# Performance work log

Hardware: AMD Instinct MI355X
Metric: run time of the kernel (lower is better)

Reference implementation:

```python
import jax, jax.numpy as jnp
import numpy as np

EPS = 1e-8

def unit_projection(x):
    # project each embedding vector so its Fourier coefficients have unit magnitude
    f = jnp.fft.fft(x, axis=-1)
    f = f / jnp.maximum(jnp.abs(f), EPS)
    return jnp.real(jnp.fft.ifft(f, axis=-1))

def bind(a, b):
    return jnp.fft.irfft(jnp.fft.rfft(a, axis=-1) * jnp.fft.rfft(b, axis=-1), n=a.shape[-1], axis=-1)

def unbind(s, k):
    # k is unit-magnitude in Fourier domain, so its inverse is its conjugate
    return jnp.fft.irfft(jnp.fft.rfft(s, axis=-1) * jnp.conj(jnp.fft.rfft(k, axis=-1)), n=s.shape[-1], axis=-1)

def layer_norm(x, g, b):
    mu = jnp.mean(x, axis=-1, keepdims=True)
    var = jnp.var(x, axis=-1, keepdims=True)
    return (x - mu) * jax.lax.rsqrt(var + 1e-5) * g + b

def setup_inputs():
    key = jax.random.key(0)
    ks = jax.random.split(key, 12)
    B, S, D = 4, 2048, 1024
    sc = 1.0 / np.sqrt(D)
    inp = {
        'x': jax.random.normal(ks[0], (B, S, D), jnp.float32),
        'Wq': jax.random.normal(ks[1], (D, D), jnp.float32) * sc,
        'bq': jnp.zeros((D,), jnp.float32),
        'Wk': jax.random.normal(ks[2], (D, D), jnp.float32) * sc,
        'bk': jnp.zeros((D,), jnp.float32),
        'Wv': jax.random.normal(ks[3], (D, D), jnp.float32) * sc,
        'bv': jnp.zeros((D,), jnp.float32),
        'ln1_g': jnp.ones((D,), jnp.float32), 'ln1_b': jnp.zeros((D,), jnp.float32),
        'ln2_g': jnp.ones((D,), jnp.float32), 'ln2_b': jnp.zeros((D,), jnp.float32),
        'W1': jax.random.normal(ks[4], (D, 4 * D), jnp.float32) * sc,
        'b1': jnp.zeros((4 * D,), jnp.float32),
        'W2': jax.random.normal(ks[5], (4 * D, D), jnp.float32) * (1.0 / np.sqrt(4 * D)),
        'b2': jnp.zeros((D,), jnp.float32),
    }
    return inp

def reference(x, Wq, bq, Wk, bk, Wv, bv, ln1_g, ln1_b, ln2_g, ln2_b, W1, b1, W2, b2):
    h = layer_norm(x, ln1_g, ln1_b)
    q = unit_projection(h @ Wq + bq)
    k = unit_projection(h @ Wk + bk)
    v = unit_projection(h @ Wv + bv)
    s = jnp.cumsum(bind(k, v), axis=1)  # causal prefix-sum over sequence
    mixed = unbind(s, q)
    x = x + mixed  # dropout=0.0
    h2 = layer_norm(x, ln2_g, ln2_b)
    mlp = jax.nn.gelu(h2 @ W1 + b1, approximate=False) @ W2 + b2
    return x + mlp
```

## Files before the change

### kernel.cpp

```cpp
#include <hip/hip_runtime.h>
#include <cstdint>
#include <cstddef>

#define DD 1024
#define SSEQ 2048
#define NB 4
#define MROWS 8192
#define FBINS 513
#define FPAD 520
#define WFP 1152
#define NQKV 3456
#define NHID 4096
#define NCHUNK 64
#define SCHUNK 32

typedef _Float16 f16_t;
typedef _Float16 f16x8 __attribute__((ext_vector_type(8)));
typedef _Float16 f16x2 __attribute__((ext_vector_type(2)));
typedef float f32x4 __attribute__((ext_vector_type(4)));

__device__ __forceinline__ float2 cmul(float2 a, float2 b) {
  return make_float2(a.x * b.x - a.y * b.y, a.x * b.y + a.y * b.x);
}

__device__ __forceinline__ void async_cp16(const void* g, void* l) {
  __builtin_amdgcn_global_load_lds(
      (const __attribute__((address_space(1))) void*)g,
      (__attribute__((address_space(3))) void*)l, 16, 0, 0);
}

template <int N> __device__ __forceinline__ void vwait();
template <> __device__ __forceinline__ void vwait<0>() { asm volatile("s_waitcnt vmcnt(0)" ::: "memory"); }
template <> __device__ __forceinline__ void vwait<1>() { asm volatile("s_waitcnt vmcnt(1)" ::: "memory"); }
template <> __device__ __forceinline__ void vwait<2>() { asm volatile("s_waitcnt vmcnt(2)" ::: "memory"); }
template <> __device__ __forceinline__ void vwait<3>() { asm volatile("s_waitcnt vmcnt(3)" ::: "memory"); }
template <> __device__ __forceinline__ void vwait<4>() { asm volatile("s_waitcnt vmcnt(4)" ::: "memory"); }

__device__ __forceinline__ float fast_gelu(float val) {
  float av = __builtin_fabsf(val);
  float z = av * 0.70710678118654752f;
  float t = __builtin_amdgcn_rcpf(__builtin_fmaf(0.3275911f, z, 1.0f));
  float poly = t * __builtin_fmaf(t,
      __builtin_fmaf(t, __builtin_fmaf(t,
          __builtin_fmaf(t, 1.061405429f, -1.453152027f),
          1.421413741f), -0.284496736f), 0.254829592f);
  float e = __builtin_amdgcn_exp2f(z * z * -1.4426950408889634f);
  float w = poly * e;
  float r = fmaxf(val, 0.0f);
  return __builtin_fmaf(-0.5f * av, w, r);
}

__device__ __forceinline__ void fft1024(float2* bufA, float2* bufB,
                                        const float2* tw, int tid) {
  float2* s = bufA;
  float2* d = bufB;
  for (int m = 1; m < 1024; m <<= 1) {
#pragma unroll
    for (int r2 = 0; r2 < 2; ++r2) {
      int u = tid + r2 * 256;
      int k = u & (m - 1);
      int jm = u - k;
      float2 c0 = s[u];
      float2 c1 = s[u + 512];
      float2 wt = tw[jm];
      float2 su = make_float2(c0.x + c1.x, c0.y + c1.y);
      float2 df = make_float2(c0.x - c1.x, c0.y - c1.y);
      float2 pr = cmul(wt, df);
      d[2 * jm + k] = su;
      d[2 * jm + k + m] = pr;
    }
    __syncthreads();
    float2* tmp = s; s = d; d = tmp;
  }
}

__device__ __forceinline__ float2* fft512(float2* bufA, float2* bufB,
                                          const float2* tw, int tid) {
  float2* s = bufA;
  float2* d = bufB;
  for (int m = 1; m < 512; m <<= 1) {
    int u = tid;
    int k = u & (m - 1);
    int jm = u - k;
    float2 c0 = s[u];
    float2 c1 = s[u + 256];
    float2 wt = tw[jm];
    float2 su = make_float2(c0.x + c1.x, c0.y + c1.y);
    float2 df = make_float2(c0.x - c1.x, c0.y - c1.y);
    float2 pr = cmul(wt, df);
    d[2 * jm + k] = su;
    d[2 * jm + k + m] = pr;
    __syncthreads();
    float2* tmp = s; s = d; d = tmp;
  }
  return s;
}

__global__ __launch_bounds__(256) void wfft_k(
    const float* __restrict__ Wq, const float* __restrict__ Wk,
    const float* __restrict__ Wv, float* __restrict__ WfAll) {
  __shared__ float2 tw[512];
  __shared__ float2 bufA[1024];
  __shared__ float2 bufB[1024];
  const int tid = threadIdx.x;
  const int p = blockIdx.x >> 10, k = blockIdx.x & 1023;
  const float* W = (p == 0) ? Wq : ((p == 1) ? Wk : Wv);
  for (int t = tid; t < 512; t += 256) {
    float ang = -6.2831853071795864769f * (float)t * (1.0f / 1024.0f);
    tw[t] = make_float2(cosf(ang), sinf(ang));
  }
  const float* src = W + (size_t)k * DD;
  for (int t = tid; t < 1024; t += 256) bufA[t] = make_float2(src[t], 0.f);
  __syncthreads();
  fft1024(bufA, bufB, tw, tid);
  float* dst = WfAll + ((size_t)p * DD + k) * WFP;
  for (int t = tid; t <= 512; t += 256) {
    float2 f = bufA[t];
    dst[2 * t] = f.x;
    dst[2 * t + 1] = f.y;
  }
  for (int j = 1026 + tid; j < WFP; j += 256) dst[j] = 0.f;
}

__global__ __launch_bounds__(256) void bfft_k(
    const float* __restrict__ bq, const float* __restrict__ bk,
    const float* __restrict__ bv, float* __restrict__ biasC) {
  __shared__ float2 tw[512];
  __shared__ float2 bufA[1024];
  __shared__ float2 bufB[1024];
  const int tid = threadIdx.x;
  const int p = blockIdx.x;
  const float* bsrc = (p == 0) ? bq : ((p == 1) ? bk : bv);
  for (int t = tid; t < 512; t += 256) {
    float ang = -6.2831853071795864769f * (float)t * (1.0f / 1024.0f);
    tw[t] = make_float2(cosf(ang), sinf(ang));
  }
  for (int t = tid; t < 1024; t += 256) bufA[t] = make_float2(bsrc[t], 0.f);
  __syncthreads();
  fft1024(bufA, bufB, tw, tid);
  float* dst = biasC + (size_t)p * WFP;
  for (int t = tid; t <= 512; t += 256) {
    float2 f = bufA[t];
    dst[2 * t] = f.x;
    dst[2 * t + 1] = f.y;
  }
  for (int j = 1026 + tid; j < WFP; j += 256) dst[j] = 0.f;
}

__global__ __launch_bounds__(256) void transpose_cast_k(
    const float* __restrict__ W, f16_t* __restrict__ Wt, int K, int N) {
  __shared__ float tile[32][33];
  const int tx = threadIdx.x & 31, ty = threadIdx.x >> 5;
  const int n0 = blockIdx.x * 32, k0 = blockIdx.y * 32;
#pragma unroll
  for (int i = 0; i < 32; i += 8)
    tile[ty + i][tx] = W[(size_t)(k0 + ty + i) * N + n0 + tx];
  __syncthreads();
#pragma unroll
  for (int i = 0; i < 32; i += 8)
    Wt[(size_t)(n0 + ty + i) * K + k0 + tx] = (f16_t)tile[tx][ty + i];
}

__global__ __launch_bounds__(256) void ln_cast2_k(
    const float* __restrict__ x, const float* __restrict__ g,
    const float* __restrict__ b, f16_t* __restrict__ hH,
    f16_t* __restrict__ hL) {
  const int row = blockIdx.x, tid = threadIdx.x;
  __shared__ float red[8];
  const float* xr = x + (size_t)row * DD;
  float v[4], ls = 0.f, lq = 0.f;
#pragma unroll
  for (int i = 0; i < 4; ++i) {
    v[i] = xr[i * 256 + tid];
    ls += v[i];
    lq += v[i] * v[i];
  }
#pragma unroll
  for (int o = 32; o > 0; o >>= 1) {
    ls += __shfl_down(ls, o);
    lq += __shfl_down(lq, o);
  }
  const int lane = tid & 63, w = tid >> 6;
  if (lane == 0) { red[w] = ls; red[w + 4] = lq; }
  __syncthreads();
  const float S = red[0] + red[1] + red[2] + red[3];
  const float Q = red[4] + red[5] + red[6] + red[7];
  const float mean = S * (1.f / 1024.f);
  const float var = Q * (1.f / 1024.f) - mean * mean;
  const float rs = rsqrtf(var + 1e-5f);
#pragma unroll
  for (int i = 0; i < 4; ++i) {
    int n = i * 256 + tid;
    float val = (v[i] - mean) * rs * g[n] + b[n];
    f16_t hi = (f16_t)val;
    hH[(size_t)row * DD + n] = hi;
    hL[(size_t)row * DD + n] = (f16_t)(val - (float)hi);
  }
}

template <int RHALF>
__device__ __forceinline__ void stage_half(const f16_t* __restrict__ G,
                                           int grow0, int ldk, int kt,
                                           f16_t* ls, int w, int lane) {
  const int srow = lane >> 3;
  const int slot = lane & 7;
#pragma unroll
  for (int j = 0; j < RHALF / 64; ++j) {
    const int rb = (w + j * 8) * 8;
    const int row = rb + srow;
    const int gg = (slot - (row & 7)) & 7;
    async_cp16(G + (size_t)(grow0 + row) * ldk + kt + gg * 8, ls + rb * 64);
  }
}

template <int BM, int BN>
__device__ __forceinline__ void readA(const f16_t* As, int mq, int wm, int lane,
                                      f16x8 (&aR)[BM / 64][2]) {
#pragma unroll
  for (int mf = 0; mf < BM / 64; ++mf) {
    const int m = mq * (BM / 2) + wm * (BM / 4) + mf * 16 + (lane & 15);
#pragma unroll
    for (int ks = 0; ks < 2; ++ks) {
      const int cg = ks * 4 + (lane >> 4);
      const int sl = (cg + (m & 7)) & 7;
      aR[mf][ks] = *(const f16x8*)(As + m * 64 + sl * 8);
    }
  }
}

template <int BM, int BN>
__device__ __forceinline__ void readB(const f16_t* Bs, int nq, int wn, int lane,
                                      f16x8 (&bR)[BN / 128][2]) {
#pragma unroll
  for (int nf = 0; nf < BN / 128; ++nf) {
    const int n = nq * (BN / 2) + wn * (BN / 8) + nf * 16 + (lane & 15);
#pragma unroll
    for (int ks = 0; ks < 2; ++ks) {
      const int cg = ks * 4 + (lane >> 4);
      const int sl = (cg + (n & 7)) & 7;
      bR[nf][ks] = *(const f16x8*)(Bs + n * 64 + sl * 8);
    }
  }
}

template <int MF, int NF>
__device__ __forceinline__ void mfma_q(f32x4 (&acc)[MF][NF],
                                       const f16x8 (&aR)[MF][2],
                                       const f16x8 (&bR)[NF][2]) {
#pragma unroll
  for (int ks = 0; ks < 2; ++ks)
#pragma unroll
    for (int mf = 0; mf < MF; ++mf)
#pragma unroll
      for (int nf = 0; nf < NF; ++nf)
        acc[mf][nf] = __builtin_amdgcn_mfma_f32_16x16x32_f16(
            aR[mf][ks], bR[nf][ks], acc[mf][nf], 0, 0, 0);
}

template <int BM, int BN, int MM, int NN, int KK, int EPI>
__global__ __launch_bounds__(512, 2) void gemm8p_k(
    const f16_t* __restrict__ A, const f16_t* __restrict__ Bt,
    const float* __restrict__ bias, const float* __restrict__ resid,
    float* __restrict__ outF, f16_t* __restrict__ outH) {
  constexpr int MF = BM / 64;
  constexpr int NF = BN / 128;
  constexpr int LA = BM / 128;
  constexpr int LB = BN / 128;
  constexpr int NT = KK / 64;
  constexpr int TILE = (BM + BN) * 64;
  __shared__ alignas(16) f16_t lds[2 * TILE];

  const int tid = threadIdx.x;
  const int lane = tid & 63;
  const int w = tid >> 6;
  const int wm = w >> 2;
  const int wn = w & 3;

  constexpr int ntm = MM / BM, ntn = NN / BN;
  constexpr int per = (ntm * ntn) / 8;
  const int lin = (int)blockIdx.x;
  const int s = (lin & 7) * per + (lin >> 3);
  const int bn = (s % ntn) * BN;
  const int bm = (s / ntn) * BM;

  f32x4 acc[2][2][MF][NF];
#pragma unroll
  for (int a0 = 0; a0 < 2; ++a0)
#pragma unroll
    for (int a1 = 0; a1 < 2; ++a1)
#pragma unroll
      for (int mf = 0; mf < MF; ++mf)
#pragma unroll
        for (int nf = 0; nf < NF; ++nf)
          acc[a0][a1][mf][nf] = (f32x4){0.f, 0.f, 0.f, 0.f};

  {
    f16_t* A0s = lds;
    f16_t* B0s = lds + BM * 64;
    stage_half<BM / 2>(A, bm, KK, 0, A0s, w, lane);
    stage_half<BN / 2>(Bt, bn, KK, 0, B0s, w, lane);
    stage_half<BN / 2>(Bt, bn + BN / 2, KK, 0, B0s + (BN / 2) * 64, w, lane);
    stage_half<BM / 2>(A, bm + BM / 2, KK, 0, A0s + (BM / 2) * 64, w, lane);
  }
  vwait<LA + LB>();
  __builtin_amdgcn_s_barrier();

  f16x8 aR[MF][2], bR0[NF][2], bR1[NF][2];

  for (int t = 0; t < NT; ++t) {
    const int cur = t & 1;
    f16_t* As = lds + cur * TILE;
    f16_t* Bs = As + BM * 64;
    f16_t* Asn = lds + (cur ^ 1) * TILE;
    f16_t* Bsn = Asn + BM * 64;
    const bool pre = (t + 1 < NT);
    const int ktn = (t + 1) << 6;

    readA<BM, BN>(As, 0, wm, lane, aR);
    readB<BM, BN>(Bs, 0, wn, lane, bR0);
    if (pre) stage_half<BM / 2>(A, bm, KK, ktn, Asn, w, lane);
    __builtin_amdgcn_s_barrier();
    __builtin_amdgcn_s_setprio(1);
    mfma_q<MF, NF>(acc[0][0], aR, bR0);
    __builtin_amdgcn_s_setprio(0);
    if (pre) vwait<2 * LA>(); else vwait<LA>();
    __builtin_amdgcn_s_barrier();

    readB<BM, BN>(Bs, 1, wn, lane, bR1);
    if (pre) stage_half<BN / 2>(Bt, bn, KK, ktn, Bsn, w, lane);
    __builtin_amdgcn_s_barrier();
    __builtin_amdgcn_s_setprio(1);
    mfma_q<MF, NF>(acc[0][1], aR, bR1);
    __builtin_amdgcn_s_setprio(0);
    if (pre) vwait<LA + LB>(); else vwait<0>();
    __builtin_amdgcn_s_barrier();

    readA<BM, BN>(As, 1, wm, lane, aR);
    if (pre) stage_half<BN / 2>(Bt, bn + BN / 2, KK, ktn,
                                Bsn + (BN / 2) * 64, w, lane);
    __builtin_amdgcn_s_barrier();
    __builtin_amdgcn_s_setprio(1);
    mfma_q<MF, NF>(acc[1][0], aR, bR0);
    __builtin_amdgcn_s_setprio(0);
    __builtin_amdgcn_s_barrier();

    if (pre) stage_half<BM / 2>(A, bm + BM / 2, KK, ktn,
                                Asn + (BM / 2) * 64, w, lane);
    __builtin_amdgcn_s_barrier();
    __builtin_amdgcn_s_setprio(1);
    mfma_q<MF, NF>(acc[1][1], aR, bR1);
    __builtin_amdgcn_s_setprio(0);
    if (pre) vwait<LA + LB>();
    __builtin_amdgcn_s_barrier();
  }

  const int q4 = lane >> 4;
  const int cn = lane & 15;
#pragma unroll
  for (int mq = 0; mq < 2; ++mq)
#pragma unroll
    for (int nq = 0; nq < 2; ++nq)
#pragma unroll
      for (int mf = 0; mf < MF; ++mf)
#pragma unroll
        for (int nf = 0; nf < NF; ++nf) {
          const int gcol = bn + nq * (BN / 2) + wn * (BN / 8) + nf * 16 + cn;
          const float bv = bias[gcol];
          const int grow0 = bm + mq * (BM / 2) + wm * (BM / 4) + mf * 16 + q4 * 4;
#pragma unroll
          for (int i = 0; i < 4; ++i) {
            const float val = acc[mq][nq][mf][nf][i] + bv;
            const size_t idx = (size_t)(grow0 + i) * NN + gcol;
            if (EPI == 1) {
              outH[idx] = (f16_t)fast_gelu(val);
            } else {
              outF[idx] = val + resid[idx];
            }
          }
        }
}

__global__ __launch_bounds__(512, 2) void gemm_qkv8p_k(
    const f16_t* __restrict__ Ahi, const f16_t* __restrict__ Alo,
    const f16_t* __restrict__ Bt, const float* __restrict__ bias,
    float* __restrict__ outF) {
  constexpr int BM = 256, BN = 128;
  constexpr int MF = 4, NF = 1;
  constexpr int LA = 2, LB = 1;
  constexpr int TILE = (BM + BN) * 64;
  __shared__ alignas(16) f16_t lds[2 * TILE];

  const int tid = threadIdx.x;
  const int lane = tid & 63;
  const int w = tid >> 6;
  const int wm = w >> 2, wn = w & 3;

  const int lin = (int)blockIdx.x;
  const int xcd = lin & 7, idx = lin >> 3;
  int bm, bn;
  bool qmode;
  if (idx < 36) {
    const int h = xcd * 36 + idx;
    bm = (h / 9) * 256;
    bn = (h % 9) * 128;
    qmode = true;
  } else {
    const int l = xcd * 72 + (idx - 36);
    bm = (l / 18) * 256;
    bn = 1152 + (l % 18) * 128;
    qmode = false;
  }
  const int NT = qmode ? 32 : 16;

  f32x4 acc[2][2][MF][NF];
#pragma unroll
  for (int a0 = 0; a0 < 2; ++a0)
#pragma unroll
    for (int a1 = 0; a1 < 2; ++a1)
#pragma unroll
      for (int mf = 0; mf < MF; ++mf)
#pragma unroll
        for (int nf = 0; nf < NF; ++nf)
          acc[a0][a1][mf][nf] = (f32x4){0.f, 0.f, 0.f, 0.f};

  {
    f16_t* A0s = lds;
    f16_t* B0s = lds + BM * 64;
    stage_half<BM / 2>(Ahi, bm, DD, 0, A0s, w, lane);
    stage_half<BN / 2>(Bt, bn, DD, 0, B0s, w, lane);
    stage_half<BN / 2>(Bt, bn + BN / 2, DD, 0, B0s + (BN / 2) * 64, w, lane);
    stage_half<BM / 2>(Ahi, bm + BM / 2, DD, 0, A0s + (BM / 2) * 64, w, lane);
  }
  vwait<LA + LB>();
  __builtin_amdgcn_s_barrier();

  f16x8 aR[MF][2], bR0[NF][2], bR1[NF][2];

  for (int t = 0; t < NT; ++t) {
    const int cur = t & 1;
    f16_t* As = lds + cur * TILE;
    f16_t* Bs = As + BM * 64;
    f16_t* Asn = lds + (cur ^ 1) * TILE;
    f16_t* Bsn = Asn + BM * 64;
    const bool pre = (t + 1 < NT);
    const int tt = t + 1;
    const f16_t* An = (qmode && tt >= 16) ? Alo : Ahi;
    const int ktn = (tt & 15) << 6;

    readA<BM, BN>(As, 0, wm, lane, aR);
    readB<BM, BN>(Bs, 0, wn, lane, bR0);
    if (pre) stage_half<BM / 2>(An, bm, DD, ktn, Asn, w, lane);
    __builtin_amdgcn_s_barrier();
    __builtin_amdgcn_s_setprio(1);
    mfma_q<MF, NF>(acc[0][0], aR, bR0);
    __builtin_amdgcn_s_setprio(0);
    if (pre) vwait<2 * LA>(); else vwait<LA>();
    __builtin_amdgcn_s_barrier();

    readB<BM, BN>(Bs, 1, wn, lane, bR1);
    if (pre) stage_half<BN / 2>(Bt, bn, DD, ktn, Bsn, w, lane);
    __builtin_amdgcn_s_barrier();
    __builtin_amdgcn_s_setprio(1);
    mfma_q<MF, NF>(acc[0][1], aR, bR1);
    __builtin_amdgcn_s_setprio(0);
    if (pre) vwait<LA + LB>(); else vwait<0>();
    __builtin_amdgcn_s_barrier();

    readA<BM, BN>(As, 1, wm, lane, aR);
    if (pre) stage_half<BN / 2>(Bt, bn + BN / 2, DD, ktn,
                                Bsn + (BN / 2) * 64, w, lane);
    __builtin_amdgcn_s_barrier();
    __builtin_amdgcn_s_setprio(1);
    mfma_q<MF, NF>(acc[1][0], aR, bR0);
    __builtin_amdgcn_s_setprio(0);
    __builtin_amdgcn_s_barrier();

    if (pre) stage_half<BM / 2>(An, bm + BM / 2, DD, ktn,
                                Asn + (BM / 2) * 64, w, lane);
    __builtin_amdgcn_s_barrier();
    __builtin_amdgcn_s_setprio(1);
    mfma_q<MF, NF>(acc[1][1], aR, bR1);
    __builtin_amdgcn_s_setprio(0);
    if (pre) vwait<LA + LB>();
    __builtin_amdgcn_s_barrier();
  }

  const int q4 = lane >> 4;
  const int cn = lane & 15;
#pragma unroll
  for (int mq = 0; mq < 2; ++mq)
#pragma unroll
    for (int nq = 0; nq < 2; ++nq)
#pragma unroll
      for (int mf = 0; mf < MF; ++mf)
#pragma unroll
        for (int nf = 0; nf < NF; ++nf) {
          const int gcol = bn + nq * (BN / 2) + wn * (BN / 8) + nf * 16 + cn;
          const float bv = bias[gcol];
          const int grow0 = bm + mq * (BM / 2) + wm * (BM / 4) + mf * 16 + q4 * 4;
#pragma unroll
          for (int i = 0; i < 4; ++i) {
            const size_t oidx = (size_t)(grow0 + i) * NQKV + gcol;
            outF[oidx] = acc[mq][nq][mf][nf][i] + bv;
          }
        }
}

__device__ __forceinline__ float2 unitc(float2 a) {
  float inv = 1.0f / fmaxf(sqrtf(a.x * a.x + a.y * a.y), 1e-8f);
  return make_float2(a.x * inv, a.y * inv);
}
__device__ __forceinline__ float2 bind_bin(const float2* r, int f) {
  float2 kn = unitc(r[576 + f]);
  float2 vn = unitc(r[1152 + f]);
  return cmul(kn, vn);
}

__global__ __launch_bounds__(256) void scan_pass1_k(
    const float* __restrict__ qkvF, float2* __restrict__ T) {
  const int bid = blockIdx.x;
  const int sc = bid & 63;
  const int fh = (bid >> 6) & 1;
  const int b = bid >> 7;
  const int s0 = sc * SCHUNK;
  const float2* base = (const float2*)(qkvF + ((size_t)(b * SSEQ + s0)) * NQKV);
  for (int f = fh * 256 + threadIdx.x; f < FBINS; f += 512) {
    float2 acc = make_float2(0.f, 0.f);
    const float2* r = base;
    for (int i = 0; i < SCHUNK; ++i) {
      float2 pv = bind_bin(r, f);
      acc.x += pv.x; acc.y += pv.y;
      r += NQKV / 2;
    }
    T[((size_t)b * NCHUNK + sc) * FBINS + f] = acc;
  }
}

__global__ void scan_pass2_k(float2* __restrict__ T) {
  const int idx = blockIdx.x * 256 + threadIdx.x;
  if (idx >= NB * FBINS) return;
  const int b = idx / FBINS, f = idx % FBINS;
  float2 acc = make_float2(0.f, 0.f);
  for (int sc = 0; sc < NCHUNK; ++sc) {
    size_t a = ((size_t)b * NCHUNK + sc) * FBINS + f;
    float2 v = T[a];
    T[a] = acc;
    acc.x += v.x; acc.y += v.y;
  }
}

__global__ __launch_bounds__(256) void scan_pass3_k(
    const float* __restrict__ qkvF, const float2* __restrict__ T,
    float2* __restrict__ Scum) {
  const int bid = blockIdx.x;
  const int sc = bid & 63;
  const int fh = (bid >> 6) & 1;
  const int b = bid >> 7;
  const int s0 = sc * SCHUNK;
  const float2* base = (const float2*)(qkvF + ((size_t)(b * SSEQ + s0)) * NQKV);
  for (int f = fh * 256 + threadIdx.x; f < FBINS; f += 512) {
    float2 acc = T[((size_t)b * NCHUNK + sc) * FBINS + f];
    const float2* r = base;
    size_t orow = ((size_t)(b * SSEQ + s0)) * FPAD + f;
    for (int i = 0; i < SCHUNK; ++i) {
      float2 pv = bind_bin(r, f);
      acc.x += pv.x; acc.y += pv.y;
      Scum[orow] = acc;
      r += NQKV / 2;
      orow += FPAD;
    }
  }
}

__global__ __launch_bounds__(256) void unbind_ln2_k(
    const float2* __restrict__ Scum, const float* __restrict__ qkvF,
    const float* __restrict__ x, float* __restrict__ x2out,
    f16_t* __restrict__ h2, const float* __restrict__ g2,
    const float* __restrict__ b2) {
  __shared__ float2 tw[256];
  __shared__ float2 Marr[513];
  __shared__ float2 bufA[512];
  __shared__ float2 bufB[512];
  __shared__ float red[8];
  const int tid = threadIdx.x;
  const int row = blockIdx.x;

  {
    float ang = 6.2831853071795864769f * (float)tid * (1.0f / 512.0f);
    tw[tid] = make_float2(cosf(ang), sinf(ang));
  }
  const float2* qrow = (const float2*)(qkvF + (size_t)row * NQKV);
  for (int t = tid; t <= 512; t += 256) {
    float2 sc = Scum[(size_t)row * FPAD + t];
    float2 fq = unitc(qrow[t]);
    Marr[t] = make_float2(sc.x * fq.x + sc.y * fq.y, sc.y * fq.x - sc.x * fq.y);
  }
  __syncthreads();
#pragma unroll
  for (int rr = 0; rr < 2; ++rr) {
    int t = tid + rr * 256;
    float2 a = Marr[t];
    float2 b = Marr[512 - t];
    float2 E = make_float2(0.5f * (a.x + b.x), 0.5f * (a.y - b.y));
    float2 Dd = make_float2(0.5f * (a.x - b.x), 0.5f * (a.y + b.y));
    float ang = 6.2831853071795864769f * (float)t * (1.0f / 1024.0f);
    float cw = cosf(ang), sw = sinf(ang);
    float2 O = make_float2(cw * Dd.x - sw * Dd.y, cw * Dd.y + sw * Dd.x);
    bufA[t] = make_float2(E.x - O.y, E.y + O.x);
  }
  __syncthreads();
  float2* res = fft512(bufA, bufB, tw, tid);

  const float* xr = x + (size_t)row * DD;
  float v[2][2];
  float ls = 0.f, lq = 0.f;
#pragma unroll
  for (int rr = 0; rr < 2; ++rr) {
    int n = tid + rr * 256;
    float2 z = res[n];
    float2 xv = *(const float2*)(xr + 2 * n);
    float v0 = xv.x + z.x * (1.0f / 512.0f);
    float v1 = xv.y + z.y * (1.0f / 512.0f);
    *(float2*)(x2out + (size_t)row * DD + 2 * n) = make_float2(v0, v1);
    v[rr][0] = v0; v[rr][1] = v1;
    ls += v0 + v1;
    lq += v0 * v0 + v1 * v1;
  }
#pragma unroll
  for (int o = 32; o > 0; o >>= 1) {
    ls += __shfl_down(ls, o);
    lq += __shfl_down(lq, o);
  }
  const int lane = tid & 63, w = tid >> 6;
  if (lane == 0) { red[w] = ls; red[w + 4] = lq; }
  __syncthreads();
  const float S = red[0] + red[1] + red[2] + red[3];
  const float Q = red[4] + red[5] + red[6] + red[7];
  const float mean = S * (1.f / 1024.f);
  const float var = Q * (1.f / 1024.f) - mean * mean;
  const float rs = rsqrtf(var + 1e-5f);
  f16_t* hr = h2 + (size_t)row * DD;
#pragma unroll
  for (int rr = 0; rr < 2; ++rr) {
    int n = tid + rr * 256;
    float2 gv = *(const float2*)(g2 + 2 * n);
    float2 bv = *(const float2*)(b2 + 2 * n);
    f16x2 hp;
    hp[0] = (f16_t)((v[rr][0] - mean) * rs * gv.x + bv.x);
    hp[1] = (f16_t)((v[rr][1] - mean) * rs * gv.y + bv.y);
    *(f16x2*)(hr + 2 * n) = hp;
  }
}

extern "C" void kernel_launch(void* const* d_in, const int* in_sizes, int n_in,
                              void* d_out, int out_size, void* d_ws,
                              size_t ws_size, hipStream_t stream) {
  const float* x     = (const float*)d_in[0];
  const float* Wq    = (const float*)d_in[1];
  const float* bq    = (const float*)d_in[2];
  const float* Wk    = (const float*)d_in[3];
  const float* bk    = (const float*)d_in[4];
  const float* Wv    = (const float*)d_in[5];
  const float* bv    = (const float*)d_in[6];
  const float* ln1_g = (const float*)d_in[7];
  const float* ln1_b = (const float*)d_in[8];
  const float* ln2_g = (const float*)d_in[9];
  const float* ln2_b = (const float*)d_in[10];
  const float* W1    = (const float*)d_in[11];
  const float* b1    = (const float*)d_in[12];
  const float* W2    = (const float*)d_in[13];
  const float* b2    = (const float*)d_in[14];
  float* out = (float*)d_out;

  char* p = (char*)d_ws;
  auto take = [&](size_t bytes) {
    char* r = p;
    p += (bytes + 255) & ~(size_t)255;
    return r;
  };
  f16_t* BtH   = (f16_t*)take((size_t)NQKV * DD * sizeof(f16_t));
  f16_t* W1T   = (f16_t*)take((size_t)NHID * DD * sizeof(f16_t));
  f16_t* W2T   = (f16_t*)take((size_t)DD * NHID * sizeof(f16_t));
  float* biasC = (float*)take((size_t)NQKV * sizeof(float));
  f16_t* hbuf  = (f16_t*)take((size_t)MROWS * DD * sizeof(f16_t));
  char*  big   = take((size_t)MROWS * NQKV * sizeof(float));
  float2* Scum = (float2*)take((size_t)MROWS * FPAD * sizeof(float2));
  float* x2    = (float*)take((size_t)MROWS * DD * sizeof(float));
  float2* Tch  = (float2*)take((size_t)NB * NCHUNK * FBINS * sizeof(float2));
  float* WfAll   = (float*)big;
  float* qkv_f   = (float*)big;
  f16_t* mlp1    = (f16_t*)big;
  f16_t* hlo     = (f16_t*)x2;

  wfft_k<<<3 * DD, 256, 0, stream>>>(Wq, Wk, Wv, WfAll);
  for (int pp = 0; pp < 3; ++pp)
    transpose_cast_k<<<dim3(WFP / 32, DD / 32), 256, 0, stream>>>(
        WfAll + (size_t)pp * DD * WFP,
        BtH + (size_t)pp * WFP * DD, DD, WFP);
  bfft_k<<<3, 256, 0, stream>>>(bq, bk, bv, biasC);
  transpose_cast_k<<<dim3(128, 32), 256, 0, stream>>>(W1, W1T, DD, NHID);
  transpose_cast_k<<<dim3(32, 128), 256, 0, stream>>>(W2, W2T, NHID, DD);

  ln_cast2_k<<<MROWS, 256, 0, stream>>>(x, ln1_g, ln1_b, hbuf, hlo);

  gemm_qkv8p_k<<<864, 512, 0, stream>>>(hbuf, hlo, BtH, biasC, qkv_f);

  scan_pass1_k<<<NB * NCHUNK * 2, 256, 0, stream>>>(qkv_f, Tch);
  scan_pass2_k<<<(NB * FBINS + 255) / 256, 256, 0, stream>>>(Tch);
  scan_pass3_k<<<NB * NCHUNK * 2, 256, 0, stream>>>(qkv_f, Tch, Scum);

  unbind_ln2_k<<<MROWS, 256, 0, stream>>>(Scum, qkv_f, x, x2, hbuf, ln2_g, ln2_b);

  gemm8p_k<256, 256, MROWS, NHID, DD, 1><<<512, 512, 0, stream>>>(
      hbuf, W1T, b1, nullptr, nullptr, mlp1);

  gemm8p_k<128, 256, MROWS, DD, NHID, 2><<<256, 512, 0, stream>>>(
      mlp1, W2T, b2, x2, out, nullptr);
}
```

Measured before the change: 520.3 us.

## Pack two rows per block in FFT kernels and restructure QKV GEMM pipeline

The weight-FFT and unbind+LayerNorm kernels now handle two rows per 512-thread block. Twiddle setup is shared between the two rows and the number of blocks is halved. The QKV GEMM main loop is reorganised from four barrier-separated phases into two. Both B fragment halves are read up front, and A/B prefetches for the next tile are issued together, which cuts barriers and waitcnt points per k-step at the cost of keeping more fragments live in registers. The larger blocks also raise shared memory use per block, which may reduce how many blocks fit on each CU.

Measured after the change: 518.2 us. No clear change (-0.4%).

```diff
diff --git a/kernel.cpp b/kernel.cpp
--- a/kernel.cpp
+++ b/kernel.cpp
@@ -51,13 +51,13 @@
 }
 
 __device__ __forceinline__ void fft1024(float2* bufA, float2* bufB,
-                                        const float2* tw, int tid) {
+                                        const float2* tw, int lt) {
   float2* s = bufA;
   float2* d = bufB;
   for (int m = 1; m < 1024; m <<= 1) {
 #pragma unroll
     for (int r2 = 0; r2 < 2; ++r2) {
-      int u = tid + r2 * 256;
+      int u = lt + r2 * 256;
       int k = u & (m - 1);
       int jm = u - k;
       float2 c0 = s[u];
@@ -75,11 +75,11 @@
 }
 
 __device__ __forceinline__ float2* fft512(float2* bufA, float2* bufB,
-                                          const float2* tw, int tid) {
+                                          const float2* tw, int lt) {
   float2* s = bufA;
   float2* d = bufB;
   for (int m = 1; m < 512; m <<= 1) {
-    int u = tid;
+    int u = lt;
     int k = u & (m - 1);
     int jm = u - k;
     float2 c0 = s[u];
@@ -96,30 +96,35 @@
   return s;
 }
 
-__global__ __launch_bounds__(256) void wfft_k(
+__global__ __launch_bounds__(512) void wfft_k(
     const float* __restrict__ Wq, const float* __restrict__ Wk,
     const float* __restrict__ Wv, float* __restrict__ WfAll) {
   __shared__ float2 tw[512];
-  __shared__ float2 bufA[1024];
-  __shared__ float2 bufB[1024];
+  __shared__ float2 bufA[2][1024];
+  __shared__ float2 bufB[2][1024];
   const int tid = threadIdx.x;
-  const int p = blockIdx.x >> 10, k = blockIdx.x & 1023;
+  const int rh = tid >> 8;
+  const int lt = tid & 255;
+  const int row = blockIdx.x * 2 + rh;
+  const int p = row >> 10, k = row & 1023;
   const float* W = (p == 0) ? Wq : ((p == 1) ? Wk : Wv);
-  for (int t = tid; t < 512; t += 256) {
-    float ang = -6.2831853071795864769f * (float)t * (1.0f / 1024.0f);
-    tw[t] = make_float2(cosf(ang), sinf(ang));
+  if (rh == 0) {
+    for (int t = lt; t < 512; t += 256) {
+      float ang = -6.2831853071795864769f * (float)t * (1.0f / 1024.0f);
+      tw[t] = make_float2(cosf(ang), sinf(ang));
+    }
   }
   const float* src = W + (size_t)k * DD;
-  for (int t = tid; t < 1024; t += 256) bufA[t] = make_float2(src[t], 0.f);
+  for (int t = lt; t < 1024; t += 256) bufA[rh][t] = make_float2(src[t], 0.f);
   __syncthreads();
-  fft1024(bufA, bufB, tw, tid);
+  fft1024(bufA[rh], bufB[rh], tw, lt);
   float* dst = WfAll + ((size_t)p * DD + k) * WFP;
-  for (int t = tid; t <= 512; t += 256) {
-    float2 f = bufA[t];
+  for (int t = lt; t <= 512; t += 256) {
+    float2 f = bufA[rh][t];
     dst[2 * t] = f.x;
     dst[2 * t + 1] = f.y;
   }
-  for (int j = 1026 + tid; j < WFP; j += 256) dst[j] = 0.f;
+  for (int j = 1026 + lt; j < WFP; j += 256) dst[j] = 0.f;
 }
 
 __global__ __launch_bounds__(256) void bfft_k(
@@ -386,7 +391,6 @@
     float* __restrict__ outF) {
   constexpr int BM = 256, BN = 128;
   constexpr int MF = 4, NF = 1;
-  constexpr int LA = 2, LB = 1;
   constexpr int TILE = (BM + BN) * 64;
   __shared__ alignas(16) f16_t lds[2 * TILE];
 
@@ -423,15 +427,10 @@
         for (int nf = 0; nf < NF; ++nf)
           acc[a0][a1][mf][nf] = (f32x4){0.f, 0.f, 0.f, 0.f};
 
-  {
-    f16_t* A0s = lds;
-    f16_t* B0s = lds + BM * 64;
-    stage_half<BM / 2>(Ahi, bm, DD, 0, A0s, w, lane);
-    stage_half<BN / 2>(Bt, bn, DD, 0, B0s, w, lane);
-    stage_half<BN / 2>(Bt, bn + BN / 2, DD, 0, B0s + (BN / 2) * 64, w, lane);
-    stage_half<BM / 2>(Ahi, bm + BM / 2, DD, 0, A0s + (BM / 2) * 64, w, lane);
-  }
-  vwait<LA + LB>();
+  stage_half<128>(Ahi, bm, DD, 0, lds, w, lane);
+  stage_half<128>(Bt, bn, DD, 0, lds + BM * 64, w, lane);
+  stage_half<128>(Ahi, bm + 128, DD, 0, lds + 128 * 64, w, lane);
+  vwait<2>();
   __builtin_amdgcn_s_barrier();
 
   f16x8 aR[MF][2], bR0[NF][2], bR1[NF][2];
@@ -449,39 +448,27 @@
 
     readA<BM, BN>(As, 0, wm, lane, aR);
     readB<BM, BN>(Bs, 0, wn, lane, bR0);
-    if (pre) stage_half<BM / 2>(An, bm, DD, ktn, Asn, w, lane);
+    readB<BM, BN>(Bs, 1, wn, lane, bR1);
+    if (pre) {
+      stage_half<128>(An, bm, DD, ktn, Asn, w, lane);
+      stage_half<128>(Bt, bn, DD, ktn, Bsn, w, lane);
+    }
     __builtin_amdgcn_s_barrier();
     __builtin_amdgcn_s_setprio(1);
     mfma_q<MF, NF>(acc[0][0], aR, bR0);
-    __builtin_amdgcn_s_setprio(0);
-    if (pre) vwait<2 * LA>(); else vwait<LA>();
-    __builtin_amdgcn_s_barrier();
-
-    readB<BM, BN>(Bs, 1, wn, lane, bR1);
-    if (pre) stage_half<BN / 2>(Bt, bn, DD, ktn, Bsn, w, lane);
-    __builtin_amdgcn_s_barrier();
-    __builtin_amdgcn_s_setprio(1);
     mfma_q<MF, NF>(acc[0][1], aR, bR1);
     __builtin_amdgcn_s_setprio(0);
-    if (pre) vwait<LA + LB>(); else vwait<0>();
+    if (pre) vwait<4>(); else vwait<0>();
     __builtin_amdgcn_s_barrier();
 
     readA<BM, BN>(As, 1, wm, lane, aR);
-    if (pre) stage_half<BN / 2>(Bt, bn + BN / 2, DD, ktn,
-                                Bsn + (BN / 2) * 64, w, lane);
+    if (pre) stage_half<128>(An, bm + 128, DD, ktn, Asn + 128 * 64, w, lane);
     __builtin_amdgcn_s_barrier();
     __builtin_amdgcn_s_setprio(1);
     mfma_q<MF, NF>(acc[1][0], aR, bR0);
-    __builtin_amdgcn_s_setprio(0);
-    __builtin_amdgcn_s_barrier();
-
-    if (pre) stage_half<BM / 2>(An, bm + BM / 2, DD, ktn,
-                                Asn + (BM / 2) * 64, w, lane);
-    __builtin_amdgcn_s_barrier();
-    __builtin_amdgcn_s_setprio(1);
     mfma_q<MF, NF>(acc[1][1], aR, bR1);
     __builtin_amdgcn_s_setprio(0);
-    if (pre) vwait<LA + LB>();
+    if (pre) vwait<2>();
     __builtin_amdgcn_s_barrier();
   }
 
@@ -572,51 +559,54 @@
   }
 }
 
-__global__ __launch_bounds__(256) void unbind_ln2_k(
+__global__ __launch_bounds__(512) void unbind_ln2_k(
     const float2* __restrict__ Scum, const float* __restrict__ qkvF,
     const float* __restrict__ x, float* __restrict__ x2out,
     f16_t* __restrict__ h2, const float* __restrict__ g2,
     const float* __restrict__ b2) {
   __shared__ float2 tw[256];
-  __shared__ float2 Marr[513];
-  __shared__ float2 bufA[512];
-  __shared__ float2 bufB[512];
-  __shared__ float red[8];
+  __shared__ float2 Marr[2][513];
+  __shared__ float2 bufA[2][512];
+  __shared__ float2 bufB[2][512];
+  __shared__ float red[2][8];
   const int tid = threadIdx.x;
-  const int row = blockIdx.x;
-
-  {
-    float ang = 6.2831853071795864769f * (float)tid * (1.0f / 512.0f);
-    tw[tid] = make_float2(cosf(ang), sinf(ang));
+  const int rh = tid >> 8;
+  const int lt = tid & 255;
+  const int row = blockIdx.x * 2 + rh;
+
+  if (rh == 0) {
+    float ang = 6.2831853071795864769f * (float)lt * (1.0f / 512.0f);
+    tw[lt] = make_float2(cosf(ang), sinf(ang));
   }
   const float2* qrow = (const float2*)(qkvF + (size_t)row * NQKV);
-  for (int t = tid; t <= 512; t += 256) {
+  for (int t = lt; t <= 512; t += 256) {
     float2 sc = Scum[(size_t)row * FPAD + t];
     float2 fq = unitc(qrow[t]);
-    Marr[t] = make_float2(sc.x * fq.x + sc.y * fq.y, sc.y * fq.x - sc.x * fq.y);
+    Marr[rh][t] = make_float2(sc.x * fq.x + sc.y * fq.y,
+                              sc.y * fq.x - sc.x * fq.y);
   }
   __syncthreads();
 #pragma unroll
   for (int rr = 0; rr < 2; ++rr) {
-    int t = tid + rr * 256;
-    float2 a = Marr[t];
-    float2 b = Marr[512 - t];
+    int t = lt + rr * 256;
+    float2 a = Marr[rh][t];
+    float2 b = Marr[rh][512 - t];
     float2 E = make_float2(0.5f * (a.x + b.x), 0.5f * (a.y - b.y));
     float2 Dd = make_float2(0.5f * (a.x - b.x), 0.5f * (a.y + b.y));
     float ang = 6.2831853071795864769f * (float)t * (1.0f / 1024.0f);
     float cw = cosf(ang), sw = sinf(ang);
     float2 O = make_float2(cw * Dd.x - sw * Dd.y, cw * Dd.y + sw * Dd.x);
-    bufA[t] = make_float2(E.x - O.y, E.y + O.x);
+    bufA[rh][t] = make_float2(E.x - O.y, E.y + O.x);
   }
   __syncthreads();
-  float2* res = fft512(bufA, bufB, tw, tid);
+  float2* res = fft512(bufA[rh], bufB[rh], tw, lt);
 
   const float* xr = x + (size_t)row * DD;
   float v[2][2];
   float ls = 0.f, lq = 0.f;
 #pragma unroll
   for (int rr = 0; rr < 2; ++rr) {
-    int n = tid + rr * 256;
+    int n = lt + rr * 256;
     float2 z = res[n];
     float2 xv = *(const float2*)(xr + 2 * n);
     float v0 = xv.x + z.x * (1.0f / 512.0f);
@@ -631,18 +621,18 @@
     ls += __shfl_down(ls, o);
     lq += __shfl_down(lq, o);
   }
-  const int lane = tid & 63, w = tid >> 6;
-  if (lane == 0) { red[w] = ls; red[w + 4] = lq; }
+  const int lane = tid & 63, w4 = (tid >> 6) & 3;
+  if (lane == 0) { red[rh][w4] = ls; red[rh][w4 + 4] = lq; }
   __syncthreads();
-  const float S = red[0] + red[1] + red[2] + red[3];
-  const float Q = red[4] + red[5] + red[6] + red[7];
+  const float S = red[rh][0] + red[rh][1] + red[rh][2] + red[rh][3];
+  const float Q = red[rh][4] + red[rh][5] + red[rh][6] + red[rh][7];
   const float mean = S * (1.f / 1024.f);
   const float var = Q * (1.f / 1024.f) - mean * mean;
   const float rs = rsqrtf(var + 1e-5f);
   f16_t* hr = h2 + (size_t)row * DD;
 #pragma unroll
   for (int rr = 0; rr < 2; ++rr) {
-    int n = tid + rr * 256;
+    int n = lt + rr * 256;
     float2 gv = *(const float2*)(g2 + 2 * n);
     float2 bv = *(const float2*)(b2 + 2 * n);
     f16x2 hp;
@@ -692,7 +682,7 @@
   f16_t* mlp1    = (f16_t*)big;
   f16_t* hlo     = (f16_t*)x2;
 
-  wfft_k<<<3 * DD, 256, 0, stream>>>(Wq, Wk, Wv, WfAll);
+  wfft_k<<<3 * DD / 2, 512, 0, stream>>>(Wq, Wk, Wv, WfAll);
   for (int pp = 0; pp < 3; ++pp)
     transpose_cast_k<<<dim3(WFP / 32, DD / 32), 256, 0, stream>>>(
         WfAll + (size_t)pp * DD * WFP,
@@ -709,7 +699,8 @@
   scan_pass2_k<<<(NB * FBINS + 255) / 256, 256, 0, stream>>>(Tch);
   scan_pass3_k<<<NB * NCHUNK * 2, 256, 0, stream>>>(qkv_f, Tch, Scum);
 
-  unbind_ln2_k<<<MROWS, 256, 0, stream>>>(Scum, qkv_f, x, x2, hbuf, ln2_g, ln2_b);
+  unbind_ln2_k<<<MROWS / 2, 512, 0, stream>>>(Scum, qkv_f, x, x2, hbuf,
+                                              ln2_g, ln2_b);
 
   gemm8p_k<256, 256, MROWS, NHID, DD, 1><<<512, 512, 0, stream>>>(
       hbuf, W1T, b1, nullptr, nullptr, mlp1);
```
